# Kernel optimization log

Hardware: AMD Instinct MI355X
Metric: run time of the kernel (lower is better)

## Reference

```python
import math
import jax, jax.numpy as jnp
import numpy as np

EMBED_DIM = 768
NUM_HEADS = 12
HEAD_DIM = EMBED_DIM // NUM_HEADS


def setup_inputs() -> dict:
    key = jax.random.key(0)
    ks = jax.random.split(key, 9)
    R, C, B, E = 128, 512, 1, EMBED_DIM
    x = jax.random.normal(ks[0], (R, C, B, E), dtype=jnp.float32)
    s = 0.02
    # weights stored so that projection is x @ W + b (i.e. torch Linear weight transposed)
    Wq = jax.random.normal(ks[1], (E, E), dtype=jnp.float32) * s
    Wk = jax.random.normal(ks[2], (E, E), dtype=jnp.float32) * s
    Wv = jax.random.normal(ks[3], (E, E), dtype=jnp.float32) * s
    Wo = jax.random.normal(ks[4], (E, E), dtype=jnp.float32) * s
    bq = jnp.zeros((E,), jnp.float32)
    bk = jnp.zeros((E,), jnp.float32)
    bv = jnp.zeros((E,), jnp.float32)
    bo = jnp.zeros((E,), jnp.float32)
    return {"x": x, "Wq": Wq, "bq": bq, "Wk": Wk, "bk": bk,
            "Wv": Wv, "bv": bv, "Wo": Wo, "bo": bo}


def reference(x, Wq, bq, Wk, bk, Wv, bv, Wo, bo):
    R, C, B, E = x.shape
    H, D = NUM_HEADS, HEAD_DIM
    # scaling = head_dim^-0.5 / sqrt(num_rows)  (align_scaling)
    scaling = (D ** -0.5) / math.sqrt(R)
    q = (x @ Wq + bq).reshape(R, C, B, H, D) * scaling
    k = (x @ Wk + bk).reshape(R, C, B, H, D)
    v = (x @ Wv + bv).reshape(R, C, B, H, D)
    # sum attention logits over rows r -> shared [h, n, i, j] attention map
    attn_weights = jnp.einsum('rinhd,rjnhd->hnij', q, k)
    attn_probs = jax.nn.softmax(attn_weights, axis=-1)
    context = jnp.einsum('hnij,rjnhd->rinhd', attn_probs, v)
    context = context.reshape(R, C, B, E)
    output = context @ Wo + bo
    return output, attn_probs
```

## Files before the change

kernel.cpp:

```cpp
#include <hip/hip_runtime.h>
#include <math.h>

#define RDIM 128
#define CDIM 512
#define EDIM 768
#define HDIM 12
#define DDIM 64
#define MDIM (RDIM*CDIM)
#define OUT_ELEMS ((size_t)MDIM*EDIM)
#define HSTRIDE ((size_t)CDIM*RDIM*DDIM)
#define WELEMS (EDIM*EDIM)

typedef unsigned short ushort_t;
typedef __attribute__((ext_vector_type(8))) short bf16x8;
typedef __attribute__((ext_vector_type(8))) unsigned short u16x8;
typedef __attribute__((ext_vector_type(4))) float f32x4;

__device__ __forceinline__ ushort_t f2bf(float f) {
    unsigned u = __float_as_uint(f);
    unsigned r = u + 0x7fffu + ((u >> 16) & 1u);
    return (ushort_t)(r >> 16);
}

__device__ __forceinline__ void gload16(const void* g, void* l) {
    __builtin_amdgcn_global_load_lds(
        (const __attribute__((address_space(1))) unsigned int*)g,
        (__attribute__((address_space(3))) unsigned int*)l, 16, 0, 0);
}

__global__ __launch_bounds__(256)
void cast_x(const float* __restrict__ x, ushort_t* __restrict__ xb) {
    size_t i = ((size_t)blockIdx.x * 256 + threadIdx.x) * 8;
    float4 a = *(const float4*)&x[i];
    float4 b = *(const float4*)&x[i + 4];
    u16x8 o;
    o[0]=f2bf(a.x); o[1]=f2bf(a.y); o[2]=f2bf(a.z); o[3]=f2bf(a.w);
    o[4]=f2bf(b.x); o[5]=f2bf(b.y); o[6]=f2bf(b.z); o[7]=f2bf(b.w);
    *(u16x8*)&xb[i] = o;
}

__global__ __launch_bounds__(256)
void transpose_cast_w(const float* __restrict__ W, ushort_t* __restrict__ Wt) {
    __shared__ ushort_t t[64][66];
    const int k0 = blockIdx.x * 64, n0 = blockIdx.y * 64;
    const int tx = threadIdx.x & 15, ty = threadIdx.x >> 4;
    #pragma unroll
    for (int rep = 0; rep < 4; ++rep) {
        int k = ty + rep * 16;
        float4 v = *(const float4*)&W[(size_t)(k0 + k) * EDIM + n0 + tx*4];
        t[k][tx*4+0] = f2bf(v.x); t[k][tx*4+1] = f2bf(v.y);
        t[k][tx*4+2] = f2bf(v.z); t[k][tx*4+3] = f2bf(v.w);
    }
    __syncthreads();
    #pragma unroll
    for (int rep = 0; rep < 4; ++rep) {
        int n = ty + rep * 16;
        ushort4 o = { t[tx*4+0][n], t[tx*4+1][n], t[tx*4+2][n], t[tx*4+3][n] };
        *(ushort4*)&Wt[(size_t)(n0 + n) * EDIM + k0 + tx*4] = o;
    }
}

__global__ __launch_bounds__(256)
void concat_bias(const float* __restrict__ bq, const float* __restrict__ bk,
                 const float* __restrict__ bv, float* __restrict__ bqkv) {
    int i = blockIdx.x * 256 + threadIdx.x;
    if (i < 768)        bqkv[i] = bq[i];
    else if (i < 1536)  bqkv[i] = bk[i - 768];
    else if (i < 2304)  bqkv[i] = bv[i - 1536];
}

#define SBAR do { __builtin_amdgcn_sched_barrier(0); \
                  __builtin_amdgcn_s_barrier(); \
                  __builtin_amdgcn_sched_barrier(0); } while(0)
#define LGKM0 do { asm volatile("s_waitcnt lgkmcnt(0)" ::: "memory"); \
                   __builtin_amdgcn_sched_barrier(0); } while(0)
#define VMCNT(n_) asm volatile("s_waitcnt vmcnt(" #n_ ")" ::: "memory")

template<int M, int N, int K, int LDK, int MODE, int NWG>
__global__ __launch_bounds__(512, 2)
void gemm8(const ushort_t* __restrict__ A, const ushort_t* __restrict__ B,
           const float* __restrict__ bias, float scale,
           float* __restrict__ outF, ushort_t* __restrict__ outB,
           size_t sAh, size_t sBh) {
    __shared__ __align__(16) char smem[131072];
    constexpr int NT = K / 64;

    const int tid = threadIdx.x;
    const int lane = tid & 63, wid = tid >> 6;
    const int fr = lane & 15, fs = lane >> 4;
    const int sw = (fr & 7) << 3;

    const int bid = blockIdx.x;
    const int w = (bid & 7) * (NWG / 8) + (bid >> 3);
    int bm, bn, h = 0, ksub = 0, plane = 0, ntile = 0;
    if (MODE == 4)      { ntile = w % 9; bm = (w / 9) * 256; bn = ntile * 256; }
    else if (MODE == 2) { plane = w >> 2; h = plane >> 2; ksub = plane & 3;
                          bm = ((w >> 1) & 1) * 256; bn = (w & 1) * 256; }
    else if (MODE == 3) { h = w >> 6; bm = ((w >> 5) & 1) * 256; bn = (w & 31) * 256; }
    else                { bm = (w / 3) * 256; bn = (w % 3) * 256; }

    const ushort_t* Ab = A + (MODE == 2 || MODE == 3 ? (size_t)h * sAh : 0)
                       + (MODE == 2 ? (size_t)ksub * 2048 : 0) + (size_t)bm * LDK;
    const ushort_t* Bb = B + (MODE == 2 || MODE == 3 ? (size_t)h * sBh : 0)
                       + (MODE == 2 ? (size_t)ksub * 2048 : 0) + (size_t)bn * LDK;

    const int r0 = tid >> 3, s0 = tid & 7;
    const size_t gO0 = (size_t)r0 * LDK + ((s0 ^ (r0 & 7)) * 8);
    const size_t gO1 = gO0 + (size_t)64 * LDK;
    const int l0 = tid * 16, l1 = tid * 16 + 8192;

#define STAGE_A(t_, h_) do { \
    char* d_ = smem + ((((t_) & 1) * 2 + (h_)) * 16384); \
    const ushort_t* s_ = Ab + (size_t)((h_) * 128) * LDK + (t_) * 64; \
    gload16(s_ + gO0, d_ + l0); gload16(s_ + gO1, d_ + l1); } while(0)
#define STAGE_B(t_, h_) do { \
    char* d_ = smem + 65536 + ((((t_) & 1) * 2 + (h_)) * 16384); \
    const ushort_t* s_ = Bb + (size_t)((h_) * 128) * LDK + (t_) * 64; \
    gload16(s_ + gO0, d_ + l0); gload16(s_ + gO1, d_ + l1); } while(0)

    f32x4 acc[16][2];
    #pragma unroll
    for (int i = 0; i < 16; ++i)
        #pragma unroll
        for (int j = 0; j < 2; ++j) acc[i][j] = (f32x4){0.f, 0.f, 0.f, 0.f};
    bf16x8 a_[4][2], b_[2][2];

#define DSREADS(t_, p_, LOADB_) do { \
    const ushort_t* As_ = (const ushort_t*)(smem + ((((t_) & 1) * 2 + ((p_) >> 1)) * 16384)); \
    _Pragma("unroll") for (int f = 0; f < 4; ++f) \
      _Pragma("unroll") for (int kk = 0; kk < 2; ++kk) \
        a_[f][kk] = *(const bf16x8*)&As_[(((p_) & 1) * 64 + f * 16 + fr) * 64 \
                                          + ((kk * 32 + fs * 8) ^ sw)]; \
    if (LOADB_) { \
      const ushort_t* Bs_ = (const ushort_t*)(smem + 65536 + ((((t_) & 1) * 2 + (wid >> 2)) * 16384)); \
      _Pragma("unroll") for (int nf = 0; nf < 2; ++nf) \
        _Pragma("unroll") for (int kk = 0; kk < 2; ++kk) \
          b_[nf][kk] = *(const bf16x8*)&Bs_[((wid & 3) * 32 + nf * 16 + fr) * 64 \
                                             + ((kk * 32 + fs * 8) ^ sw)]; } } while(0)

#define MFMA16(p_) do { \
    __builtin_amdgcn_s_setprio(1); \
    _Pragma("unroll") for (int f = 0; f < 4; ++f) \
      _Pragma("unroll") for (int nf = 0; nf < 2; ++nf) \
        _Pragma("unroll") for (int kk = 0; kk < 2; ++kk) \
          acc[(p_) * 4 + f][nf] = __builtin_amdgcn_mfma_f32_16x16x32_bf16( \
              a_[f][kk], b_[nf][kk], acc[(p_) * 4 + f][nf], 0, 0, 0); \
    __builtin_amdgcn_s_setprio(0); } while(0)

    STAGE_B(0, 0); __builtin_amdgcn_sched_barrier(0);
    STAGE_B(0, 1); __builtin_amdgcn_sched_barrier(0);
    STAGE_A(0, 0); __builtin_amdgcn_sched_barrier(0);
    STAGE_A(0, 1); __builtin_amdgcn_sched_barrier(0);
    STAGE_B(1, 0); __builtin_amdgcn_sched_barrier(0);
    STAGE_B(1, 1); __builtin_amdgcn_sched_barrier(0);
    STAGE_A(1, 0); __builtin_amdgcn_sched_barrier(0);
    VMCNT(8);
    SBAR;

    for (int t = 0; t < NT - 2; ++t) {
        DSREADS(t, 0, 1);
        STAGE_A(t + 1, 1);
        SBAR; LGKM0; MFMA16(0); SBAR;
        DSREADS(t, 1, 0);
        STAGE_B(t + 2, 0);
        VMCNT(10);
        SBAR; LGKM0; MFMA16(1); SBAR;
        DSREADS(t, 2, 0);
        STAGE_B(t + 2, 1);
        SBAR; LGKM0; MFMA16(2); SBAR;
        DSREADS(t, 3, 0);
        STAGE_A(t + 2, 0);
        VMCNT(8);
        SBAR; LGKM0; MFMA16(3); SBAR;
    }

    STAGE_A(NT - 1, 1);
    VMCNT(0);
    SBAR;
    {
        constexpr int t0 = NT - 2;
        #pragma unroll
        for (int p = 0; p < 4; ++p) {
            DSREADS(t0, p, p == 0);
            SBAR; LGKM0; MFMA16(p); SBAR;
        }
        constexpr int t1 = NT - 1;
        #pragma unroll
        for (int p = 0; p < 4; ++p) {
            DSREADS(t1, p, p == 0);
            SBAR; LGKM0; MFMA16(p); SBAR;
        }
    }

    if (MODE == 4) {
        const int which = ntile / 3;
        const int hcb = (ntile % 3) * 256;
        if (which < 2) {
            ushort_t* dst = outB + (size_t)which * OUT_ELEMS;
            const float sc = (which == 0) ? scale : 1.f;
            #pragma unroll
            for (int mf = 0; mf < 16; ++mf) {
                #pragma unroll
                for (int nf = 0; nf < 2; ++nf) {
                    const int hcol = hcb + wid*32 + nf*16 + fr;
                    const float bv = bias[which*768 + hcol];
                    const int hh = hcol >> 6, d = hcol & 63;
                    #pragma unroll
                    for (int j = 0; j < 4; ++j) {
                        const int m = bm + mf*16 + fs*4 + j;
                        float v = (acc[mf][nf][j] + bv) * sc;
                        size_t addr = (size_t)hh * HSTRIDE
                                    + (size_t)(m & 511) * 8192 + (m >> 9) * 64 + d;
                        dst[addr] = f2bf(v);
                    }
                }
            }
        } else {
            ushort_t* Ts = (ushort_t*)smem;
            ushort_t* dst = outB + 2 * OUT_ELEMS;
            const int rblk = bm >> 9, jb = bm & 511;
            __syncthreads();
            #pragma unroll
            for (int q = 0; q < 2; ++q) {
                if ((wid >> 2) == q) {
                    #pragma unroll
                    for (int mf = 0; mf < 16; ++mf) {
                        #pragma unroll
                        for (int nf = 0; nf < 2; ++nf) {
                            const int nl = wid*32 + nf*16 + fr;
                            const float bv = bias[1536 + hcb + nl];
                            #pragma unroll
                            for (int j = 0; j < 4; ++j)
                                Ts[(nl & 127)*258 + mf*16 + fs*4 + j] =
                                    f2bf(acc[mf][nf][j] + bv);
                        }
                    }
                }
                __syncthreads();
                #pragma unroll
                for (int it = 0; it < 8; ++it) {
                    const int idx = it * 512 + tid;
                    const int row = idx >> 5, c8 = (idx & 31) * 8;
                    const int nl = q*128 + row;
                    const int hh = (hcb + nl) >> 6, d = nl & 63;
                    uint4 wv;
                    wv.x = *(const uint*)&Ts[row*258 + c8];
                    wv.y = *(const uint*)&Ts[row*258 + c8 + 2];
                    wv.z = *(const uint*)&Ts[row*258 + c8 + 4];
                    wv.w = *(const uint*)&Ts[row*258 + c8 + 6];
                    size_t addr = (size_t)hh * HSTRIDE
                                + (size_t)(rblk*64 + d) * CDIM + jb + c8;
                    *(uint4*)&dst[addr] = wv;
                }
                __syncthreads();
            }
        }
        return;
    }

    #pragma unroll
    for (int mf = 0; mf < 16; ++mf) {
        #pragma unroll
        for (int nf = 0; nf < 2; ++nf) {
            const int n = bn + wid*32 + nf*16 + fr;
            float bv = (MODE == 1) ? bias[n] : 0.f;
            #pragma unroll
            for (int j = 0; j < 4; ++j) {
                const int m = bm + mf*16 + fs*4 + j;
                float v = acc[mf][nf][j];
                if (MODE == 1) {
                    outF[(size_t)m * N + n] = v + bv;
                } else if (MODE == 2) {
                    outF[(size_t)plane * (CDIM*CDIM) + (size_t)m * CDIM + n] = v;
                } else {
                    size_t addr = ((size_t)(n >> 6) * CDIM + m) * EDIM
                                + h * DDIM + (n & 63);
                    outB[addr] = f2bf(v);
                }
            }
        }
    }
}

__global__ __launch_bounds__(256)
void softmax_reduce(const float* __restrict__ part, float* __restrict__ attn,
                    ushort_t* __restrict__ Pb) {
    const int row = blockIdx.x;
    const int h = row >> 9, c = row & 511;
    const int tid = threadIdx.x;
    const int lane = tid & 63, wid = tid >> 6;
    __shared__ float red[8];

    float v0 = 0.f, v1 = 0.f;
    #pragma unroll
    for (int s = 0; s < 4; ++s) {
        const float* p = part + ((size_t)(h*4 + s) * (CDIM*CDIM)) + (size_t)c * CDIM;
        v0 += p[tid];
        v1 += p[tid + 256];
    }
    float m = fmaxf(v0, v1);
    #pragma unroll
    for (int off = 32; off > 0; off >>= 1) m = fmaxf(m, __shfl_down(m, off));
    if (lane == 0) red[wid] = m;
    __syncthreads();
    if (tid == 0) red[4] = fmaxf(fmaxf(red[0], red[1]), fmaxf(red[2], red[3]));
    __syncthreads();
    const float M = red[4];

    float e0 = expf(v0 - M), e1 = expf(v1 - M);
    float s = e0 + e1;
    #pragma unroll
    for (int off = 32; off > 0; off >>= 1) s += __shfl_down(s, off);
    __syncthreads();
    if (lane == 0) red[wid] = s;
    __syncthreads();
    if (tid == 0) red[5] = red[0] + red[1] + red[2] + red[3];
    __syncthreads();
    const float inv = 1.f / red[5];
    float o0 = e0 * inv, o1 = e1 * inv;
    float* pout = attn + (size_t)row * CDIM;
    ushort_t* pb = Pb + (size_t)row * CDIM;
    pout[tid] = o0;        pout[tid + 256] = o1;
    pb[tid]   = f2bf(o0);  pb[tid + 256]   = f2bf(o1);
}

extern "C" void kernel_launch(void* const* d_in, const int* in_sizes, int n_in,
                              void* d_out, int out_size, void* d_ws, size_t ws_size,
                              hipStream_t stream) {
    const float* x  = (const float*)d_in[0];
    const float* Wq = (const float*)d_in[1];
    const float* bq = (const float*)d_in[2];
    const float* Wk = (const float*)d_in[3];
    const float* bk = (const float*)d_in[4];
    const float* Wv = (const float*)d_in[5];
    const float* bv = (const float*)d_in[6];
    const float* Wo = (const float*)d_in[7];
    const float* bo = (const float*)d_in[8];

    float* out   = (float*)d_out;
    float* attnp = out + OUT_ELEMS;

    ushort_t* ws   = (ushort_t*)d_ws;
    ushort_t* xb   = ws;
    ushort_t* Wqkv = xb + OUT_ELEMS;
    ushort_t* Wto  = Wqkv + 3*WELEMS;
    float*    bqkv = (float*)(Wto + WELEMS);
    ushort_t* Qp   = Wto + WELEMS + 4608;
    ushort_t* Kp   = Qp + OUT_ELEMS;
    ushort_t* Vt   = Kp + OUT_ELEMS;
    ushort_t* Pb   = Vt + OUT_ELEMS;
    float*    part = (float*)(Pb + (size_t)HDIM*CDIM*CDIM);
    ushort_t* ctxb = xb;

    const float scaling = 0.011048543456039806f;

    cast_x<<<MDIM*EDIM/(256*8), 256, 0, stream>>>(x, xb);
    dim3 wt(EDIM/64, EDIM/64);
    transpose_cast_w<<<wt, 256, 0, stream>>>(Wq, Wqkv);
    transpose_cast_w<<<wt, 256, 0, stream>>>(Wk, Wqkv + WELEMS);
    transpose_cast_w<<<wt, 256, 0, stream>>>(Wv, Wqkv + 2*WELEMS);
    transpose_cast_w<<<wt, 256, 0, stream>>>(Wo, Wto);
    concat_bias<<<9, 256, 0, stream>>>(bq, bk, bv, bqkv);

    gemm8<MDIM, 2304, EDIM, EDIM, 4, 2304><<<2304, 512, 0, stream>>>(
        xb, Wqkv, bqkv, scaling, nullptr, Qp, 0, 0);

    gemm8<CDIM, CDIM, 2048, 8192, 2, 192><<<192, 512, 0, stream>>>(
        Qp, Kp, nullptr, 1.f, part, nullptr, HSTRIDE, HSTRIDE);

    softmax_reduce<<<HDIM*CDIM, 256, 0, stream>>>(part, attnp, Pb);

    gemm8<CDIM, 8192, CDIM, CDIM, 3, 768><<<768, 512, 0, stream>>>(
        Pb, Vt, nullptr, 1.f, nullptr, ctxb, (size_t)CDIM*CDIM, HSTRIDE);

    gemm8<MDIM, EDIM, EDIM, EDIM, 1, 768><<<768, 512, 0, stream>>>(
        ctxb, Wto, bo, 1.f, out, nullptr, 0, 0);
}
```

Baseline: 608.7 us.

## Retile GEMM warps to a 2x4 grid with 128x64 per-wave tiles

Changes each wave's output tile from 256x32 to 128x64 by arranging the 8 waves as 2 rows by 4 columns, with the A and B fragment loads reworked to match. Each wave now reads half as much A from LDS per k-step while reading more B, which cuts total LDS read traffic. The main loop is reorganized into four MFMA phases per k-tile with fewer barriers, and both A halves of the next tile are staged together. The transpose scratch pitch also changes from 258 to 264. The deeper prefetch changes the vmcnt accounting and the new schedule has fewer points that hide latency, so correctness and overlap depend on the new wait counts.

```diff
diff --git a/kernel.cpp b/kernel.cpp
--- a/kernel.cpp
+++ b/kernel.cpp
@@ -87,6 +87,7 @@
 
     const int tid = threadIdx.x;
     const int lane = tid & 63, wid = tid >> 6;
+    const int wr = wid >> 2, wc = wid & 3;
     const int fr = lane & 15, fs = lane >> 4;
     const int sw = (fr & 7) << 3;
 
@@ -118,33 +119,34 @@
     const ushort_t* s_ = Bb + (size_t)((h_) * 128) * LDK + (t_) * 64; \
     gload16(s_ + gO0, d_ + l0); gload16(s_ + gO1, d_ + l1); } while(0)
 
-    f32x4 acc[16][2];
-    #pragma unroll
-    for (int i = 0; i < 16; ++i)
+    f32x4 acc[8][4];
+    #pragma unroll
+    for (int i = 0; i < 8; ++i)
         #pragma unroll
-        for (int j = 0; j < 2; ++j) acc[i][j] = (f32x4){0.f, 0.f, 0.f, 0.f};
-    bf16x8 a_[4][2], b_[2][2];
-
-#define DSREADS(t_, p_, LOADB_) do { \
-    const ushort_t* As_ = (const ushort_t*)(smem + ((((t_) & 1) * 2 + ((p_) >> 1)) * 16384)); \
+        for (int j = 0; j < 4; ++j) acc[i][j] = (f32x4){0.f, 0.f, 0.f, 0.f};
+    bf16x8 a_[4][2], bb_[4][2];
+
+#define DSA(t_, mq_) do { \
+    const ushort_t* As_ = (const ushort_t*)(smem + ((((t_) & 1) * 2 + wr) * 16384)); \
     _Pragma("unroll") for (int f = 0; f < 4; ++f) \
       _Pragma("unroll") for (int kk = 0; kk < 2; ++kk) \
-        a_[f][kk] = *(const bf16x8*)&As_[(((p_) & 1) * 64 + f * 16 + fr) * 64 \
-                                          + ((kk * 32 + fs * 8) ^ sw)]; \
-    if (LOADB_) { \
-      const ushort_t* Bs_ = (const ushort_t*)(smem + 65536 + ((((t_) & 1) * 2 + (wid >> 2)) * 16384)); \
-      _Pragma("unroll") for (int nf = 0; nf < 2; ++nf) \
-        _Pragma("unroll") for (int kk = 0; kk < 2; ++kk) \
-          b_[nf][kk] = *(const bf16x8*)&Bs_[((wid & 3) * 32 + nf * 16 + fr) * 64 \
-                                             + ((kk * 32 + fs * 8) ^ sw)]; } } while(0)
-
-#define MFMA16(p_) do { \
+        a_[f][kk] = *(const bf16x8*)&As_[((mq_) * 64 + f * 16 + fr) * 64 \
+                                          + ((kk * 32 + fs * 8) ^ sw)]; } while(0)
+
+#define DSB(t_) do { \
+    const ushort_t* Bs_ = (const ushort_t*)(smem + 65536 + ((((t_) & 1) * 2 + (wc >> 1)) * 16384)); \
+    _Pragma("unroll") for (int nf = 0; nf < 4; ++nf) \
+      _Pragma("unroll") for (int kk = 0; kk < 2; ++kk) \
+        bb_[nf][kk] = *(const bf16x8*)&Bs_[((wc & 1) * 64 + nf * 16 + fr) * 64 \
+                                            + ((kk * 32 + fs * 8) ^ sw)]; } while(0)
+
+#define MFMA8(mq_, nq_) do { \
     __builtin_amdgcn_s_setprio(1); \
     _Pragma("unroll") for (int f = 0; f < 4; ++f) \
-      _Pragma("unroll") for (int nf = 0; nf < 2; ++nf) \
+      _Pragma("unroll") for (int nf2 = 0; nf2 < 2; ++nf2) \
         _Pragma("unroll") for (int kk = 0; kk < 2; ++kk) \
-          acc[(p_) * 4 + f][nf] = __builtin_amdgcn_mfma_f32_16x16x32_bf16( \
-              a_[f][kk], b_[nf][kk], acc[(p_) * 4 + f][nf], 0, 0, 0); \
+          acc[(mq_) * 4 + f][(nq_) * 2 + nf2] = __builtin_amdgcn_mfma_f32_16x16x32_bf16( \
+              a_[f][kk], bb_[(nq_) * 2 + nf2][kk], acc[(mq_) * 4 + f][(nq_) * 2 + nf2], 0, 0, 0); \
     __builtin_amdgcn_s_setprio(0); } while(0)
 
     STAGE_B(0, 0); __builtin_amdgcn_sched_barrier(0);
@@ -154,42 +156,34 @@
     STAGE_B(1, 0); __builtin_amdgcn_sched_barrier(0);
     STAGE_B(1, 1); __builtin_amdgcn_sched_barrier(0);
     STAGE_A(1, 0); __builtin_amdgcn_sched_barrier(0);
+    STAGE_A(1, 1); __builtin_amdgcn_sched_barrier(0);
     VMCNT(8);
     SBAR;
 
     for (int t = 0; t < NT - 2; ++t) {
-        DSREADS(t, 0, 1);
-        STAGE_A(t + 1, 1);
-        SBAR; LGKM0; MFMA16(0); SBAR;
-        DSREADS(t, 1, 0);
+        DSA(t, 0); DSB(t);
+        LGKM0; MFMA8(0, 0); SBAR;
         STAGE_B(t + 2, 0);
-        VMCNT(10);
-        SBAR; LGKM0; MFMA16(1); SBAR;
-        DSREADS(t, 2, 0);
+        MFMA8(0, 1); SBAR;
+        DSA(t, 1);
         STAGE_B(t + 2, 1);
-        SBAR; LGKM0; MFMA16(2); SBAR;
-        DSREADS(t, 3, 0);
-        STAGE_A(t + 2, 0);
+        LGKM0; MFMA8(1, 0); SBAR;
+        STAGE_A(t + 2, 0); STAGE_A(t + 2, 1);
+        MFMA8(1, 1);
         VMCNT(8);
-        SBAR; LGKM0; MFMA16(3); SBAR;
-    }
-
-    STAGE_A(NT - 1, 1);
-    VMCNT(0);
-    SBAR;
-    {
-        constexpr int t0 = NT - 2;
-        #pragma unroll
-        for (int p = 0; p < 4; ++p) {
-            DSREADS(t0, p, p == 0);
-            SBAR; LGKM0; MFMA16(p); SBAR;
-        }
-        constexpr int t1 = NT - 1;
-        #pragma unroll
-        for (int p = 0; p < 4; ++p) {
-            DSREADS(t1, p, p == 0);
-            SBAR; LGKM0; MFMA16(p); SBAR;
-        }
+        SBAR;
+    }
+
+    #pragma unroll
+    for (int tt = 0; tt < 2; ++tt) {
+        const int t = NT - 2 + tt;
+        if (tt == 1) { VMCNT(0); SBAR; }
+        DSA(t, 0); DSB(t);
+        LGKM0; MFMA8(0, 0); SBAR;
+        MFMA8(0, 1); SBAR;
+        DSA(t, 1);
+        LGKM0; MFMA8(1, 0); SBAR;
+        MFMA8(1, 1); SBAR;
     }
 
     if (MODE == 4) {
@@ -199,15 +193,15 @@
             ushort_t* dst = outB + (size_t)which * OUT_ELEMS;
             const float sc = (which == 0) ? scale : 1.f;
             #pragma unroll
-            for (int mf = 0; mf < 16; ++mf) {
+            for (int mf = 0; mf < 8; ++mf) {
                 #pragma unroll
-                for (int nf = 0; nf < 2; ++nf) {
-                    const int hcol = hcb + wid*32 + nf*16 + fr;
+                for (int nf = 0; nf < 4; ++nf) {
+                    const int hcol = hcb + wc*64 + nf*16 + fr;
                     const float bv = bias[which*768 + hcol];
                     const int hh = hcol >> 6, d = hcol & 63;
                     #pragma unroll
                     for (int j = 0; j < 4; ++j) {
-                        const int m = bm + mf*16 + fs*4 + j;
+                        const int m = bm + wr*128 + mf*16 + fs*4 + j;
                         float v = (acc[mf][nf][j] + bv) * sc;
                         size_t addr = (size_t)hh * HSTRIDE
                                     + (size_t)(m & 511) * 8192 + (m >> 9) * 64 + d;
@@ -222,16 +216,16 @@
             __syncthreads();
             #pragma unroll
             for (int q = 0; q < 2; ++q) {
-                if ((wid >> 2) == q) {
+                if ((wc >> 1) == q) {
                     #pragma unroll
-                    for (int mf = 0; mf < 16; ++mf) {
+                    for (int mf = 0; mf < 8; ++mf) {
                         #pragma unroll
-                        for (int nf = 0; nf < 2; ++nf) {
-                            const int nl = wid*32 + nf*16 + fr;
+                        for (int nf = 0; nf < 4; ++nf) {
+                            const int nl = wc*64 + nf*16 + fr;
                             const float bv = bias[1536 + hcb + nl];
                             #pragma unroll
                             for (int j = 0; j < 4; ++j)
-                                Ts[(nl & 127)*258 + mf*16 + fs*4 + j] =
+                                Ts[(nl & 127)*264 + wr*128 + mf*16 + fs*4 + j] =
                                     f2bf(acc[mf][nf][j] + bv);
                         }
                     }
@@ -244,10 +238,10 @@
                     const int nl = q*128 + row;
                     const int hh = (hcb + nl) >> 6, d = nl & 63;
                     uint4 wv;
-                    wv.x = *(const uint*)&Ts[row*258 + c8];
-                    wv.y = *(const uint*)&Ts[row*258 + c8 + 2];
-                    wv.z = *(const uint*)&Ts[row*258 + c8 + 4];
-                    wv.w = *(const uint*)&Ts[row*258 + c8 + 6];
+                    wv.x = *(const uint*)&Ts[row*264 + c8];
+                    wv.y = *(const uint*)&Ts[row*264 + c8 + 2];
+                    wv.z = *(const uint*)&Ts[row*264 + c8 + 4];
+                    wv.w = *(const uint*)&Ts[row*264 + c8 + 6];
                     size_t addr = (size_t)hh * HSTRIDE
                                 + (size_t)(rblk*64 + d) * CDIM + jb + c8;
                     *(uint4*)&dst[addr] = wv;
@@ -259,14 +253,14 @@
     }
 
     #pragma unroll
-    for (int mf = 0; mf < 16; ++mf) {
+    for (int mf = 0; mf < 8; ++mf) {
         #pragma unroll
-        for (int nf = 0; nf < 2; ++nf) {
-            const int n = bn + wid*32 + nf*16 + fr;
+        for (int nf = 0; nf < 4; ++nf) {
+            const int n = bn + wc*64 + nf*16 + fr;
             float bv = (MODE == 1) ? bias[n] : 0.f;
             #pragma unroll
             for (int j = 0; j < 4; ++j) {
-                const int m = bm + mf*16 + fs*4 + j;
+                const int m = bm + wr*128 + mf*16 + fs*4 + j;
                 float v = acc[mf][nf][j];
                 if (MODE == 1) {
                     outF[(size_t)m * N + n] = v + bv;
```

Measured after the change: 587.8 us. 1.04x faster.
